# Performance work log

Hardware: AMD Instinct MI355X
Metric: run time of the kernel (lower is better)

## Reference

```python
import jax, jax.numpy as jnp
import numpy as np

KH, KW = 3, 3
STRIDE = 1
PADDING = 1
CIN, COUT = 64, 64


def setup_inputs() -> dict:
    key = jax.random.key(0)
    kx, kw, kb = jax.random.split(key, 3)
    x = jax.random.normal(kx, (16, CIN, 112, 112), dtype=jnp.float32)
    # Kaiming-uniform style init, matching the torch module
    fan = CIN * KH * KW
    gain = np.sqrt(2.0)
    bound_w = np.sqrt(3.0) * gain / np.sqrt(fan)
    weights = jax.random.uniform(kw, (COUT, CIN, KH, KW), dtype=jnp.float32,
                                 minval=-bound_w, maxval=bound_w)
    bound_b = 1.0 / np.sqrt(fan)
    bias = jax.random.uniform(kb, (COUT,), dtype=jnp.float32,
                              minval=-bound_b, maxval=bound_b)
    return {"x": x, "weights": weights, "bias": bias}


def reference(x, weights, bias):
    # Equivalent to F.unfold + GEMM: a standard cross-correlation conv.
    # x: (N, C, H, W), weights: (F, C, KH, KW) -> out: (N, F, H', W')
    out = jax.lax.conv_general_dilated(
        x, weights,
        window_strides=(STRIDE, STRIDE),
        padding=((PADDING, PADDING), (PADDING, PADDING)),
        dimension_numbers=("NCHW", "OIHW", "NCHW"),
    )
    return out + bias[None, :, None, None]
```

## Files before the change

### kernel.cpp

```cpp
#include <hip/hip_runtime.h>


typedef __attribute__((ext_vector_type(8))) short bf16x8;
typedef __attribute__((ext_vector_type(4))) float f32x4;

#define CIN 64
#define COUT 64
#define HH 112
#define WW 112
#define ROWS 4
#define DYS  6

#define XP 72
#define WCOLS 114
#define LDS_SHORTS (DYS * WCOLS * XP)

__device__ __forceinline__ unsigned short f2bf(float f) {
    unsigned u = __builtin_bit_cast(unsigned, f);
    u += 0x7FFFu + ((u >> 16) & 1u);
    return (unsigned short)(u >> 16);
}

__global__ void conv_wprep(const float* __restrict__ w, short* __restrict__ wbf) {
    int i = blockIdx.x * 256 + threadIdx.x;
    int j = i & 7;
    int f = (i >> 3) & 63;
    int koct = (i >> 9) & 3;
    int cb = (i >> 11) & 1;
    int t = i >> 12;
    int c = cb * 32 + koct * 8 + j;
    int ky = t / 3, kx = t - ky * 3;
    wbf[i] = (short)f2bf(w[((f * CIN + c) * 3 + ky) * 3 + kx]);
}

__global__ __launch_bounds__(256, 1)
void conv3x3_mfma(const float* __restrict__ x, const short* __restrict__ wbf,
                  const float* __restrict__ bias, float* __restrict__ out)
{
    __shared__ __align__(16) short lds[LDS_SHORTS];
    const int tid = threadIdx.x;
    const int n = blockIdx.x;
    const int h0 = blockIdx.y * ROWS;

    const int wave = tid >> 6;
    const int lane = tid & 63;
    const int lm = lane & 15;
    const int q  = lane >> 4;

    if (tid < 192) {
        int e = tid & 15;
        int g = tid >> 4;
        int dy = g >> 1;
        int wcol = (g & 1) ? (WCOLS - 1) : 0;
        *(uint2*)&lds[((dy * WCOLS + wcol) * 36 + e * 2) * 2] = (uint2){0u, 0u};
    }
    if (h0 == 0) {
        for (int i = tid; i < WCOLS * 16; i += 256) {
            int wcol = i >> 4, e = i & 15;
            *(uint2*)&lds[((0 * WCOLS + wcol) * 36 + e * 2) * 2] = (uint2){0u, 0u};
        }
    }
    if (h0 == HH - ROWS) {
        for (int i = tid; i < WCOLS * 16; i += 256) {
            int wcol = i >> 4, e = i & 15;
            *(uint2*)&lds[((5 * WCOLS + wcol) * 36 + e * 2) * 2] = (uint2){0u, 0u};
        }
    }
    for (int i = tid; i < DYS * 16 * 28; i += 256) {
        int w4 = i % 28;
        int rp = i / 28;
        int dy = rp >> 4;
        int cq = rp & 15;
        int gh = h0 + dy - 1;
        if ((unsigned)gh < (unsigned)HH) {
            int c = cq * 4;
            const float* px = x + (((n * CIN + c) * HH + gh) * WW + w4 * 4);
            const float4 v0 = *(const float4*)px;
            const float4 v1 = *(const float4*)(px + HH * WW);
            const float4 v2 = *(const float4*)(px + 2 * HH * WW);
            const float4 v3 = *(const float4*)(px + 3 * HH * WW);
            int o = cq >> 1, p = cq & 1;
            float a0[4] = {v0.x, v0.y, v0.z, v0.w};
            float a1[4] = {v1.x, v1.y, v1.z, v1.w};
            float a2[4] = {v2.x, v2.y, v2.z, v2.w};
            float a3[4] = {v3.x, v3.y, v3.z, v3.w};
#pragma unroll
            for (int dw = 0; dw < 4; ++dw) {
                int wcol = 1 + w4 * 4 + dw;
                int swz = (wcol >> 2) & 7;
                int dslot = 4 * (o ^ swz) + 2 * p;
                uint2 pk;
                pk.x = (unsigned)f2bf(a0[dw]) | ((unsigned)f2bf(a1[dw]) << 16);
                pk.y = (unsigned)f2bf(a2[dw]) | ((unsigned)f2bf(a3[dw]) << 16);
                *(uint2*)&lds[((dy * WCOLS + wcol) * 36 + dslot) * 2] = pk;
            }
        }
    }

    bf16x8 br[2][4][2];
#pragma unroll
    for (int nt = 0; nt < 4; ++nt) {
        br[0][nt][0] = *(const bf16x8*)(wbf + (0 * 8 + q) * 512 + (nt * 16 + lm) * 8);
        br[0][nt][1] = *(const bf16x8*)(wbf + (0 * 8 + 4 + q) * 512 + (nt * 16 + lm) * 8);
    }

    __syncthreads();

    f32x4 acc[7][4];
#pragma unroll
    for (int mt = 0; mt < 7; ++mt)
#pragma unroll
        for (int nt = 0; nt < 4; ++nt) acc[mt][nt] = (f32x4){0.f, 0.f, 0.f, 0.f};

#pragma unroll
    for (int t = 0; t < 9; ++t) {
        const int buf = t & 1;
        if (t < 8) {
#pragma unroll
            for (int nt = 0; nt < 4; ++nt) {
                br[1 - buf][nt][0] = *(const bf16x8*)(wbf + ((t + 1) * 8 + q) * 512 + (nt * 16 + lm) * 8);
                br[1 - buf][nt][1] = *(const bf16x8*)(wbf + ((t + 1) * 8 + 4 + q) * 512 + (nt * 16 + lm) * 8);
            }
        }
        const int ky = t / 3, kx = t - ky * 3;
#pragma unroll
        for (int mt = 0; mt < 7; ++mt) {
            int wcol = mt * 16 + lm + kx;
            int swz = (wcol >> 2) & 7;
            int base = ((wave + ky) * WCOLS + wcol) * XP;
            bf16x8 a0 = *(const bf16x8*)&lds[base + 8 * (q ^ swz)];
            bf16x8 a1 = *(const bf16x8*)&lds[base + 8 * ((q + 4) ^ swz)];
#pragma unroll
            for (int nt = 0; nt < 4; ++nt)
                acc[mt][nt] = __builtin_amdgcn_mfma_f32_16x16x32_bf16(a0, br[buf][nt][0], acc[mt][nt], 0, 0, 0);
#pragma unroll
            for (int nt = 0; nt < 4; ++nt)
                acc[mt][nt] = __builtin_amdgcn_mfma_f32_16x16x32_bf16(a1, br[buf][nt][1], acc[mt][nt], 0, 0, 0);
        }
    }

    float* lout = (float*)lds;
#pragma unroll
    for (int pass = 0; pass < 2; ++pass) {
        __syncthreads();
#pragma unroll
        for (int mt = 0; mt < 7; ++mt)
#pragma unroll
            for (int ntl = 0; ntl < 2; ++ntl) {
                const f32x4 v = acc[mt][pass * 2 + ntl];
#pragma unroll
                for (int r = 0; r < 4; ++r)
                    lout[(wave * 32 + ntl * 16 + lm) * 113 + mt * 16 + q * 4 + r] = v[r];
            }
        __syncthreads();
        for (int i = tid; i < 128 * 28; i += 256) {
            int fr = i / 28;
            int w4 = i - fr * 28;
            int w = fr >> 5;
            int f = pass * 32 + (fr & 31);
            float b = bias[f];
            const float* lp = lout + fr * 113 + w4 * 4;
            float4 v;
            v.x = lp[0] + b; v.y = lp[1] + b; v.z = lp[2] + b; v.w = lp[3] + b;
            *(float4*)(out + (((n * COUT + f) * HH + h0 + w) * WW + w4 * 4)) = v;
        }
    }
}

extern "C" void kernel_launch(void* const* d_in, const int* in_sizes, int n_in,
                              void* d_out, int out_size, void* d_ws, size_t ws_size,
                              hipStream_t stream) {
    const float* x = (const float*)d_in[0];
    const float* w = (const float*)d_in[1];
    const float* b = (const float*)d_in[2];
    float* out = (float*)d_out;
    short* wbf = (short*)d_ws;

    conv_wprep<<<144, 256, 0, stream>>>(w, wbf);
    dim3 grid(16, HH / ROWS);
    conv3x3_mfma<<<grid, 256, 0, stream>>>(x, wbf, b, out);
}
```

Baseline: 130.1 us.

## Halve rows per block, split output channels across waves, target two blocks per CU

Each block now computes 2 output rows instead of 4. The four waves are split as 2 rows × 2 output-channel halves, so each wave holds half the accumulators and weight registers. This lets launch bounds request 2 blocks per CU, doubles the grid, and shrinks LDS per block so two blocks can co-reside. The epilogue collapses to a single pass, and the bf16 packing uses a hardware packed-convert builtin when available. The cost is more redundant halo loading, since 4 input rows are staged per 2 output rows instead of 6 per 4, and each A fragment is reused across fewer MFMAs.

```diff
diff --git a/kernel.cpp b/kernel.cpp
--- a/kernel.cpp
+++ b/kernel.cpp
@@ -8,8 +8,8 @@
 #define COUT 64
 #define HH 112
 #define WW 112
-#define ROWS 4
-#define DYS  6
+#define ROWS 2
+#define DYS  4
 
 #define XP 72
 #define WCOLS 114
@@ -20,6 +20,18 @@
     u += 0x7FFFu + ((u >> 16) & 1u);
     return (unsigned short)(u >> 16);
 }
+
+#if __has_builtin(__builtin_amdgcn_cvt_pk_bf16_f32)
+__device__ __forceinline__ unsigned pk2bf(float a, float b) {
+    typedef __attribute__((ext_vector_type(2))) __bf16 bf16x2;
+    bf16x2 r = __builtin_amdgcn_cvt_pk_bf16_f32(a, b);
+    return __builtin_bit_cast(unsigned, r);
+}
+#else
+__device__ __forceinline__ unsigned pk2bf(float a, float b) {
+    return (unsigned)f2bf(a) | ((unsigned)f2bf(b) << 16);
+}
+#endif
 
 __global__ void conv_wprep(const float* __restrict__ w, short* __restrict__ wbf) {
     int i = blockIdx.x * 256 + threadIdx.x;
@@ -33,7 +45,7 @@
     wbf[i] = (short)f2bf(w[((f * CIN + c) * 3 + ky) * 3 + kx]);
 }
 
-__global__ __launch_bounds__(256, 1)
+__global__ __launch_bounds__(256, 2)
 void conv3x3_mfma(const float* __restrict__ x, const short* __restrict__ wbf,
                   const float* __restrict__ bias, float* __restrict__ out)
 {
@@ -43,11 +55,13 @@
     const int h0 = blockIdx.y * ROWS;
 
     const int wave = tid >> 6;
+    const int r  = wave >> 1;
+    const int nh = wave & 1;
     const int lane = tid & 63;
     const int lm = lane & 15;
     const int q  = lane >> 4;
 
-    if (tid < 192) {
+    if (tid < 128) {
         int e = tid & 15;
         int g = tid >> 4;
         int dy = g >> 1;
@@ -63,7 +77,7 @@
     if (h0 == HH - ROWS) {
         for (int i = tid; i < WCOLS * 16; i += 256) {
             int wcol = i >> 4, e = i & 15;
-            *(uint2*)&lds[((5 * WCOLS + wcol) * 36 + e * 2) * 2] = (uint2){0u, 0u};
+            *(uint2*)&lds[(((DYS - 1) * WCOLS + wcol) * 36 + e * 2) * 2] = (uint2){0u, 0u};
         }
     }
     for (int i = tid; i < DYS * 16 * 28; i += 256) {
@@ -90,36 +104,38 @@
                 int swz = (wcol >> 2) & 7;
                 int dslot = 4 * (o ^ swz) + 2 * p;
                 uint2 pk;
-                pk.x = (unsigned)f2bf(a0[dw]) | ((unsigned)f2bf(a1[dw]) << 16);
-                pk.y = (unsigned)f2bf(a2[dw]) | ((unsigned)f2bf(a3[dw]) << 16);
+                pk.x = pk2bf(a0[dw], a1[dw]);
+                pk.y = pk2bf(a2[dw], a3[dw]);
                 *(uint2*)&lds[((dy * WCOLS + wcol) * 36 + dslot) * 2] = pk;
             }
         }
     }
 
-    bf16x8 br[2][4][2];
+    bf16x8 br[2][2][2];
 #pragma unroll
-    for (int nt = 0; nt < 4; ++nt) {
-        br[0][nt][0] = *(const bf16x8*)(wbf + (0 * 8 + q) * 512 + (nt * 16 + lm) * 8);
-        br[0][nt][1] = *(const bf16x8*)(wbf + (0 * 8 + 4 + q) * 512 + (nt * 16 + lm) * 8);
+    for (int ntl = 0; ntl < 2; ++ntl) {
+        int f = (nh * 2 + ntl) * 16 + lm;
+        br[0][ntl][0] = *(const bf16x8*)(wbf + (q) * 512 + f * 8);
+        br[0][ntl][1] = *(const bf16x8*)(wbf + (4 + q) * 512 + f * 8);
     }
 
     __syncthreads();
 
-    f32x4 acc[7][4];
+    f32x4 acc[7][2];
 #pragma unroll
     for (int mt = 0; mt < 7; ++mt)
 #pragma unroll
-        for (int nt = 0; nt < 4; ++nt) acc[mt][nt] = (f32x4){0.f, 0.f, 0.f, 0.f};
+        for (int ntl = 0; ntl < 2; ++ntl) acc[mt][ntl] = (f32x4){0.f, 0.f, 0.f, 0.f};
 
 #pragma unroll
     for (int t = 0; t < 9; ++t) {
         const int buf = t & 1;
         if (t < 8) {
 #pragma unroll
-            for (int nt = 0; nt < 4; ++nt) {
-                br[1 - buf][nt][0] = *(const bf16x8*)(wbf + ((t + 1) * 8 + q) * 512 + (nt * 16 + lm) * 8);
-                br[1 - buf][nt][1] = *(const bf16x8*)(wbf + ((t + 1) * 8 + 4 + q) * 512 + (nt * 16 + lm) * 8);
+            for (int ntl = 0; ntl < 2; ++ntl) {
+                int f = (nh * 2 + ntl) * 16 + lm;
+                br[1 - buf][ntl][0] = *(const bf16x8*)(wbf + ((t + 1) * 8 + q) * 512 + f * 8);
+                br[1 - buf][ntl][1] = *(const bf16x8*)(wbf + ((t + 1) * 8 + 4 + q) * 512 + f * 8);
             }
         }
         const int ky = t / 3, kx = t - ky * 3;
@@ -127,43 +143,41 @@
         for (int mt = 0; mt < 7; ++mt) {
             int wcol = mt * 16 + lm + kx;
             int swz = (wcol >> 2) & 7;
-            int base = ((wave + ky) * WCOLS + wcol) * XP;
+            int base = ((r + ky) * WCOLS + wcol) * XP;
             bf16x8 a0 = *(const bf16x8*)&lds[base + 8 * (q ^ swz)];
             bf16x8 a1 = *(const bf16x8*)&lds[base + 8 * ((q + 4) ^ swz)];
 #pragma unroll
-            for (int nt = 0; nt < 4; ++nt)
-                acc[mt][nt] = __builtin_amdgcn_mfma_f32_16x16x32_bf16(a0, br[buf][nt][0], acc[mt][nt], 0, 0, 0);
+            for (int ntl = 0; ntl < 2; ++ntl)
+                acc[mt][ntl] = __builtin_amdgcn_mfma_f32_16x16x32_bf16(a0, br[buf][ntl][0], acc[mt][ntl], 0, 0, 0);
 #pragma unroll
-            for (int nt = 0; nt < 4; ++nt)
-                acc[mt][nt] = __builtin_amdgcn_mfma_f32_16x16x32_bf16(a1, br[buf][nt][1], acc[mt][nt], 0, 0, 0);
+            for (int ntl = 0; ntl < 2; ++ntl)
+                acc[mt][ntl] = __builtin_amdgcn_mfma_f32_16x16x32_bf16(a1, br[buf][ntl][1], acc[mt][ntl], 0, 0, 0);
         }
     }
 
+    __syncthreads();
     float* lout = (float*)lds;
 #pragma unroll
-    for (int pass = 0; pass < 2; ++pass) {
-        __syncthreads();
+    for (int mt = 0; mt < 7; ++mt)
 #pragma unroll
-        for (int mt = 0; mt < 7; ++mt)
+        for (int ntl = 0; ntl < 2; ++ntl) {
+            const f32x4 v = acc[mt][ntl];
+            int fr = r * 64 + (nh * 2 + ntl) * 16 + lm;
 #pragma unroll
-            for (int ntl = 0; ntl < 2; ++ntl) {
-                const f32x4 v = acc[mt][pass * 2 + ntl];
-#pragma unroll
-                for (int r = 0; r < 4; ++r)
-                    lout[(wave * 32 + ntl * 16 + lm) * 113 + mt * 16 + q * 4 + r] = v[r];
-            }
-        __syncthreads();
-        for (int i = tid; i < 128 * 28; i += 256) {
-            int fr = i / 28;
-            int w4 = i - fr * 28;
-            int w = fr >> 5;
-            int f = pass * 32 + (fr & 31);
-            float b = bias[f];
-            const float* lp = lout + fr * 113 + w4 * 4;
-            float4 v;
-            v.x = lp[0] + b; v.y = lp[1] + b; v.z = lp[2] + b; v.w = lp[3] + b;
-            *(float4*)(out + (((n * COUT + f) * HH + h0 + w) * WW + w4 * 4)) = v;
+            for (int rr = 0; rr < 4; ++rr)
+                lout[fr * 113 + mt * 16 + q * 4 + rr] = v[rr];
         }
+    __syncthreads();
+    for (int i = tid; i < 128 * 28; i += 256) {
+        int fr = i / 28;
+        int w4 = i - fr * 28;
+        int rw = fr >> 6;
+        int f = fr & 63;
+        float b = bias[f];
+        const float* lp = lout + fr * 113 + w4 * 4;
+        float4 v;
+        v.x = lp[0] + b; v.y = lp[1] + b; v.z = lp[2] + b; v.w = lp[3] + b;
+        *(float4*)(out + (((n * COUT + f) * HH + h0 + rw) * WW + w4 * 4)) = v;
     }
 }
 
```

Measured after the change: 123.9 us. 1.05x faster.
